# Performance work log

Measured on AMD Instinct MI355X. Metric: run time of the kernel, lower is better.

The kernel has to match this reference:

```python
import jax, jax.numpy as jnp
import numpy as np

INPUT, HIDDEN, OUTPUT = 128, 256, 128
BATCH, SEQ = 128, 2048


def setup_inputs() -> dict:
    key = jax.random.key(0)
    ks = jax.random.split(key, 6)
    s_in = 1.0 / np.sqrt(INPUT)
    s_h = 1.0 / np.sqrt(HIDDEN)
    return {
        "x": jax.random.normal(ks[0], (BATCH, SEQ, INPUT), dtype=jnp.float32),
        "W_in": jax.random.uniform(ks[1], (HIDDEN, INPUT), jnp.float32, -s_in, s_in),
        "b_in": jax.random.uniform(ks[2], (HIDDEN,), jnp.float32, -s_in, s_in),
        "W_rec": jax.random.uniform(ks[3], (HIDDEN, HIDDEN), jnp.float32, -s_h, s_h),
        "W_out": jax.random.uniform(ks[4], (OUTPUT, HIDDEN), jnp.float32, -s_h, s_h),
        "b_out": jax.random.uniform(ks[5], (OUTPUT,), jnp.float32, -s_h, s_h),
    }


def reference(x, W_in, b_in, W_rec, W_out, b_out):
    # Precompute input projection for all timesteps in one big GEMM: [B,S,H]
    xin = jnp.einsum("bsi,hi->bsh", x, W_in) + b_in

    def step(h, xin_t):
        # h: [B,H]; xin_t: [B,H]
        h_new = jax.nn.sigmoid(xin_t + h @ W_rec.T)
        return h_new, None

    h0 = jnp.zeros((x.shape[0], W_rec.shape[0]), dtype=x.dtype)
    h_final, _ = jax.lax.scan(step, h0, jnp.swapaxes(xin, 0, 1))  # scan over seq
    return h_final @ W_out.T + b_out  # [B, OUTPUT]
```

## Files before the change

kernel.cpp:

```cpp
#include <hip/hip_runtime.h>
#include <hip/hip_bf16.h>


#define BATCH 128
#define SEQ   2048
#define NIN   128
#define NH    256
#define NOUT  128

#define BTILE 16
#define NBLK  (BATCH / BTILE)
#define HPITCH 264
#define XPITCH 136
#define TCHUNK 16
#define LOG2E 1.4426950408889634f

typedef __attribute__((ext_vector_type(8))) short short8;
typedef __attribute__((ext_vector_type(4))) float f32x4;

__device__ __forceinline__ ushort f2bf(float f) {
    union { float f; uint u; } v; v.f = f;
    uint r = v.u + 0x7fffu + ((v.u >> 16) & 1u);
    return (ushort)(r >> 16);
}

__device__ __forceinline__ uint pk_bf16(float a, float b) {
    float2 p; p.x = a; p.y = b;
    __hip_bfloat162 h = __float22bfloat162_rn(p);
    union { __hip_bfloat162 h; uint u; } v; v.h = h; return v.u;
}

__device__ __forceinline__ short8 load_wfrag_s(const float* __restrict__ W, int ld,
                                               int row, int col, float scale) {
    const float4* p = (const float4*)(W + (size_t)row * ld + col);
    float4 a = p[0], b = p[1];
    union { short8 v; ushort u[8]; } r;
    r.u[0] = f2bf(a.x * scale); r.u[1] = f2bf(a.y * scale);
    r.u[2] = f2bf(a.z * scale); r.u[3] = f2bf(a.w * scale);
    r.u[4] = f2bf(b.x * scale); r.u[5] = f2bf(b.y * scale);
    r.u[6] = f2bf(b.z * scale); r.u[7] = f2bf(b.w * scale);
    return r.v;
}

__device__ __forceinline__ float bfhi2f(uint u) {
    union { uint u; float f; } v; v.u = u & 0xffff0000u; return v.f;
}
__device__ __forceinline__ float bflo2f(uint u) {
    union { uint u; float f; } v; v.u = u << 16; return v.f;
}

__global__ __launch_bounds__(256, 1)
void xin_gemm(const float* __restrict__ x,
              const float* __restrict__ W_in,
              const float* __restrict__ b_in,
              ushort* __restrict__ xin) {
    const int tid  = threadIdx.x;
    const int lane = tid & 63;
    const int wid  = tid >> 6;
    const int n15  = lane & 15;
    const int q    = lane >> 4;
    const int bblk = blockIdx.x * BTILE;
    const int t0   = blockIdx.y * TCHUNK;

    short8 win[4][4];
    float  bias[4][4];
    #pragma unroll
    for (int mt = 0; mt < 4; ++mt) {
        const int row = (wid * 4 + mt) * 16 + n15;
        #pragma unroll
        for (int kt = 0; kt < 4; ++kt)
            win[mt][kt] = load_wfrag_s(W_in, NIN, row, kt * 32 + q * 8, LOG2E);
        #pragma unroll
        for (int r = 0; r < 4; ++r)
            bias[mt][r] = LOG2E * b_in[(wid * 4 + mt) * 16 + q * 4 + r];
    }

    const size_t xrow = (size_t)(bblk + n15) * SEQ * NIN;

    #pragma unroll 1
    for (int tt = 0; tt < TCHUNK; ++tt) {
        const int t = t0 + tt;
        short8 bx[4];
        #pragma unroll
        for (int kt = 0; kt < 4; ++kt) {
            const float4* p = (const float4*)(x + xrow + (size_t)t * NIN + kt * 32 + q * 8);
            float4 a = p[0], b = p[1];
            union { short8 v; ushort u[8]; } r;
            r.u[0] = f2bf(a.x); r.u[1] = f2bf(a.y); r.u[2] = f2bf(a.z); r.u[3] = f2bf(a.w);
            r.u[4] = f2bf(b.x); r.u[5] = f2bf(b.y); r.u[6] = f2bf(b.z); r.u[7] = f2bf(b.w);
            bx[kt] = r.v;
        }
        f32x4 acc[4];
        #pragma unroll
        for (int mt = 0; mt < 4; ++mt) {
            acc[mt][0] = bias[mt][0]; acc[mt][1] = bias[mt][1];
            acc[mt][2] = bias[mt][2]; acc[mt][3] = bias[mt][3];
        }
        #pragma unroll
        for (int kt = 0; kt < 4; ++kt)
            #pragma unroll
            for (int mt = 0; mt < 4; ++mt)
                acc[mt] = __builtin_amdgcn_mfma_f32_16x16x32_bf16(
                    win[mt][kt], bx[kt], acc[mt], 0, 0, 0);
        #pragma unroll
        for (int mt = 0; mt < 4; ++mt) {
            uint2 w;
            w.x = pk_bf16(acc[mt][0], acc[mt][1]);
            w.y = pk_bf16(acc[mt][2], acc[mt][3]);
            *(uint2*)&xin[(size_t)t * BATCH * NH + (size_t)(bblk + n15) * NH
                          + (wid * 4 + mt) * 16 + q * 4] = w;
        }
    }
}

__global__ __launch_bounds__(512, 2)
void elman_scan(const ushort* __restrict__ xin,
                const float* __restrict__ W_rec,
                const float* __restrict__ W_out,
                const float* __restrict__ b_out,
                float* __restrict__ out) {
    const int tid  = threadIdx.x;
    const int lane = tid & 63;
    const int wid  = tid >> 6;
    const int n15  = lane & 15;
    const int q    = lane >> 4;
    const int bblk = blockIdx.x * BTILE;

    __shared__ __align__(16) ushort hlds[2][BTILE * HPITCH];

    short8 wrec[2][8];
    #pragma unroll
    for (int mt = 0; mt < 2; ++mt) {
        const int row = (wid * 2 + mt) * 16 + n15;
        #pragma unroll
        for (int kt = 0; kt < 8; ++kt)
            wrec[mt][kt] = load_wfrag_s(W_rec, NH, row, kt * 32 + q * 8, LOG2E);
    }

    for (int i = tid; i < BTILE * HPITCH / 2; i += 512)
        ((uint*)hlds[0])[i] = 0u;

    const size_t xoff = (size_t)(bblk + n15) * NH + q * 4;
    uint2 xin_cur[2], xin_nxt[2];
    #pragma unroll
    for (int mt = 0; mt < 2; ++mt)
        xin_cur[mt] = *(const uint2*)&xin[xoff + (wid * 2 + mt) * 16];

    __syncthreads();

    #pragma unroll 1
    for (int t = 0; t < SEQ; ++t) {
        const int cur = t & 1, nxt = cur ^ 1;

        const int tp = (t + 1 < SEQ) ? (t + 1) : (SEQ - 1);
        const size_t pb = (size_t)tp * BATCH * NH + xoff;
        #pragma unroll
        for (int mt = 0; mt < 2; ++mt)
            xin_nxt[mt] = *(const uint2*)&xin[pb + (wid * 2 + mt) * 16];

        short8 bh[8];
        #pragma unroll
        for (int kt = 0; kt < 8; ++kt)
            bh[kt] = *(const short8*)&hlds[cur][n15 * HPITCH + kt * 32 + q * 8];

        f32x4 acc[2];
        #pragma unroll
        for (int mt = 0; mt < 2; ++mt) {
            acc[mt][0] = bflo2f(xin_cur[mt].x);
            acc[mt][1] = bfhi2f(xin_cur[mt].x);
            acc[mt][2] = bflo2f(xin_cur[mt].y);
            acc[mt][3] = bfhi2f(xin_cur[mt].y);
        }
        #pragma unroll
        for (int kt = 0; kt < 8; ++kt)
            #pragma unroll
            for (int mt = 0; mt < 2; ++mt)
                acc[mt] = __builtin_amdgcn_mfma_f32_16x16x32_bf16(
                    wrec[mt][kt], bh[kt], acc[mt], 0, 0, 0);

        #pragma unroll
        for (int mt = 0; mt < 2; ++mt) {
            float h0 = __builtin_amdgcn_rcpf(1.0f + __builtin_amdgcn_exp2f(-acc[mt][0]));
            float h1 = __builtin_amdgcn_rcpf(1.0f + __builtin_amdgcn_exp2f(-acc[mt][1]));
            float h2 = __builtin_amdgcn_rcpf(1.0f + __builtin_amdgcn_exp2f(-acc[mt][2]));
            float h3 = __builtin_amdgcn_rcpf(1.0f + __builtin_amdgcn_exp2f(-acc[mt][3]));
            uint2 w;
            w.x = pk_bf16(h0, h1);
            w.y = pk_bf16(h2, h3);
            *(uint2*)&hlds[nxt][n15 * HPITCH + (wid * 2 + mt) * 16 + q * 4] = w;
        }

        #pragma unroll
        for (int mt = 0; mt < 2; ++mt) xin_cur[mt] = xin_nxt[mt];

        __syncthreads();
    }

    short8 wout[8];
    float  bo[4];
    {
        const int row = wid * 16 + n15;
        #pragma unroll
        for (int kt = 0; kt < 8; ++kt)
            wout[kt] = load_wfrag_s(W_out, NH, row, kt * 32 + q * 8, 1.0f);
        #pragma unroll
        for (int r = 0; r < 4; ++r)
            bo[r] = b_out[wid * 16 + q * 4 + r];
    }
    f32x4 oacc;
    oacc[0] = bo[0]; oacc[1] = bo[1]; oacc[2] = bo[2]; oacc[3] = bo[3];
    #pragma unroll
    for (int kt = 0; kt < 8; ++kt) {
        short8 bh = *(const short8*)&hlds[0][n15 * HPITCH + kt * 32 + q * 8];
        oacc = __builtin_amdgcn_mfma_f32_16x16x32_bf16(wout[kt], bh, oacc, 0, 0, 0);
    }
    #pragma unroll
    for (int r = 0; r < 4; ++r) {
        const int o = wid * 16 + q * 4 + r;
        out[(size_t)(bblk + n15) * NOUT + o] = oacc[r];
    }
}

__global__ __launch_bounds__(256, 1)
void elman_mfma(const float* __restrict__ x,
                const float* __restrict__ W_in,
                const float* __restrict__ b_in,
                const float* __restrict__ W_rec,
                const float* __restrict__ W_out,
                const float* __restrict__ b_out,
                float* __restrict__ out) {
    const int tid  = threadIdx.x;
    const int lane = tid & 63;
    const int wid  = tid >> 6;
    const int n15  = lane & 15;
    const int q    = lane >> 4;
    const int bblk = blockIdx.x * BTILE;

    __shared__ __align__(16) ushort hlds[2][BTILE * HPITCH];
    __shared__ __align__(16) ushort xlds[2][BTILE * XPITCH];

    short8 wrec[4][8];
    short8 win[4][4];
    float  bias[4][4];
    #pragma unroll
    for (int mt = 0; mt < 4; ++mt) {
        const int row = (wid * 4 + mt) * 16 + n15;
        #pragma unroll
        for (int kt = 0; kt < 8; ++kt)
            wrec[mt][kt] = load_wfrag_s(W_rec, NH, row, kt * 32 + q * 8, 1.0f);
        #pragma unroll
        for (int kt = 0; kt < 4; ++kt)
            win[mt][kt] = load_wfrag_s(W_in, NIN, row, kt * 32 + q * 8, 1.0f);
        #pragma unroll
        for (int r = 0; r < 4; ++r)
            bias[mt][r] = b_in[(wid * 4 + mt) * 16 + q * 4 + r];
    }

    for (int i = tid; i < BTILE * HPITCH / 2; i += 256)
        ((uint*)hlds[0])[i] = 0u;

    const int xr = tid >> 4;
    const int xc = (tid & 15) * 8;
    const size_t xbase = ((size_t)(bblk + xr)) * SEQ * NIN + xc;
    {
        const float4* p = (const float4*)(x + xbase);
        float4 a = p[0], b = p[1];
        union { uint4 u4; ushort s[8]; } px;
        px.s[0] = f2bf(a.x); px.s[1] = f2bf(a.y); px.s[2] = f2bf(a.z); px.s[3] = f2bf(a.w);
        px.s[4] = f2bf(b.x); px.s[5] = f2bf(b.y); px.s[6] = f2bf(b.z); px.s[7] = f2bf(b.w);
        *(uint4*)&xlds[0][xr * XPITCH + xc] = px.u4;
    }
    __syncthreads();

    #pragma unroll 1
    for (int t = 0; t < SEQ; ++t) {
        const int cur = t & 1, nxt = cur ^ 1;
        float4 xp0{}, xp1{};
        if (t + 1 < SEQ) {
            const float4* p = (const float4*)(x + xbase + (size_t)(t + 1) * NIN);
            xp0 = p[0]; xp1 = p[1];
        }
        short8 bx[4], bh[8];
        #pragma unroll
        for (int kt = 0; kt < 4; ++kt)
            bx[kt] = *(const short8*)&xlds[cur][n15 * XPITCH + kt * 32 + q * 8];
        #pragma unroll
        for (int kt = 0; kt < 8; ++kt)
            bh[kt] = *(const short8*)&hlds[cur][n15 * HPITCH + kt * 32 + q * 8];
        f32x4 acc[4];
        #pragma unroll
        for (int mt = 0; mt < 4; ++mt) {
            acc[mt][0] = bias[mt][0]; acc[mt][1] = bias[mt][1];
            acc[mt][2] = bias[mt][2]; acc[mt][3] = bias[mt][3];
        }
        #pragma unroll
        for (int kt = 0; kt < 4; ++kt)
            #pragma unroll
            for (int mt = 0; mt < 4; ++mt)
                acc[mt] = __builtin_amdgcn_mfma_f32_16x16x32_bf16(
                    win[mt][kt], bx[kt], acc[mt], 0, 0, 0);
        #pragma unroll
        for (int kt = 0; kt < 8; ++kt)
            #pragma unroll
            for (int mt = 0; mt < 4; ++mt)
                acc[mt] = __builtin_amdgcn_mfma_f32_16x16x32_bf16(
                    wrec[mt][kt], bh[kt], acc[mt], 0, 0, 0);
        #pragma unroll
        for (int mt = 0; mt < 4; ++mt) {
            float h0 = 1.0f / (1.0f + __expf(-acc[mt][0]));
            float h1 = 1.0f / (1.0f + __expf(-acc[mt][1]));
            float h2 = 1.0f / (1.0f + __expf(-acc[mt][2]));
            float h3 = 1.0f / (1.0f + __expf(-acc[mt][3]));
            uint2 w;
            w.x = pk_bf16(h0, h1);
            w.y = pk_bf16(h2, h3);
            *(uint2*)&hlds[nxt][n15 * HPITCH + (wid * 4 + mt) * 16 + q * 4] = w;
        }
        if (t + 1 < SEQ) {
            union { uint4 u4; ushort s[8]; } px;
            px.s[0] = f2bf(xp0.x); px.s[1] = f2bf(xp0.y);
            px.s[2] = f2bf(xp0.z); px.s[3] = f2bf(xp0.w);
            px.s[4] = f2bf(xp1.x); px.s[5] = f2bf(xp1.y);
            px.s[6] = f2bf(xp1.z); px.s[7] = f2bf(xp1.w);
            *(uint4*)&xlds[nxt][xr * XPITCH + xc] = px.u4;
        }
        __syncthreads();
    }

    short8 wout[2][8];
    float  bo[2][4];
    #pragma unroll
    for (int mo = 0; mo < 2; ++mo) {
        const int row = (wid * 2 + mo) * 16 + n15;
        #pragma unroll
        for (int kt = 0; kt < 8; ++kt)
            wout[mo][kt] = load_wfrag_s(W_out, NH, row, kt * 32 + q * 8, 1.0f);
        #pragma unroll
        for (int r = 0; r < 4; ++r)
            bo[mo][r] = b_out[(wid * 2 + mo) * 16 + q * 4 + r];
    }
    f32x4 oacc[2];
    #pragma unroll
    for (int mo = 0; mo < 2; ++mo) {
        oacc[mo][0] = bo[mo][0]; oacc[mo][1] = bo[mo][1];
        oacc[mo][2] = bo[mo][2]; oacc[mo][3] = bo[mo][3];
    }
    #pragma unroll
    for (int kt = 0; kt < 8; ++kt) {
        short8 bh = *(const short8*)&hlds[0][n15 * HPITCH + kt * 32 + q * 8];
        #pragma unroll
        for (int mo = 0; mo < 2; ++mo)
            oacc[mo] = __builtin_amdgcn_mfma_f32_16x16x32_bf16(
                wout[mo][kt], bh, oacc[mo], 0, 0, 0);
    }
    #pragma unroll
    for (int mo = 0; mo < 2; ++mo)
        #pragma unroll
        for (int r = 0; r < 4; ++r) {
            const int o = (wid * 2 + mo) * 16 + q * 4 + r;
            out[(size_t)(bblk + n15) * NOUT + o] = oacc[mo][r];
        }
}

extern "C" void kernel_launch(void* const* d_in, const int* in_sizes, int n_in,
                              void* d_out, int out_size, void* d_ws, size_t ws_size,
                              hipStream_t stream) {
    const float* x     = (const float*)d_in[0];
    const float* W_in  = (const float*)d_in[1];
    const float* b_in  = (const float*)d_in[2];
    const float* W_rec = (const float*)d_in[3];
    const float* W_out = (const float*)d_in[4];
    const float* b_out = (const float*)d_in[5];
    float* out = (float*)d_out;

    const size_t need = (size_t)SEQ * BATCH * NH * sizeof(ushort);
    if (ws_size >= need) {
        ushort* xin = (ushort*)d_ws;
        dim3 g1(NBLK, SEQ / TCHUNK);
        xin_gemm<<<g1, 256, 0, stream>>>(x, W_in, b_in, xin);
        elman_scan<<<NBLK, 512, 0, stream>>>(xin, W_rec, W_out, b_out, out);
    } else {
        elman_mfma<<<NBLK, 256, 0, stream>>>(x, W_in, b_in, W_rec, W_out, b_out, out);
    }
}
```

Baseline: 1.463 ms.

## Store xin in fragment-native layout and shrink scan block to four waves

The input-projection kernel now stages x through LDS with coalesced row loads and a double buffer. It writes xin in an MFMA-fragment-ordered layout so each lane of the scan kernel reads one contiguous uint2 per tile. The scan kernel drops from 8 to 4 waves per block, each owning 4 output tiles, which makes the per-step barrier cheaper. It also prefetches xin two steps ahead and replaces __syncthreads with a raw lgkmcnt wait plus s_barrier. In exchange, each wave does more serial MFMA work per step and holds more registers for W_rec fragments.

```diff
diff --git a/kernel.cpp b/kernel.cpp
--- a/kernel.cpp
+++ b/kernel.cpp
@@ -53,7 +53,7 @@
 void xin_gemm(const float* __restrict__ x,
               const float* __restrict__ W_in,
               const float* __restrict__ b_in,
-              ushort* __restrict__ xin) {
+              uint2* __restrict__ xin) {
     const int tid  = threadIdx.x;
     const int lane = tid & 63;
     const int wid  = tid >> 6;
@@ -62,6 +62,8 @@
     const int bblk = blockIdx.x * BTILE;
     const int t0   = blockIdx.y * TCHUNK;
 
+    __shared__ __align__(16) ushort xlds[2][BTILE * XPITCH];
+
     short8 win[4][4];
     float  bias[4][4];
     #pragma unroll
@@ -75,21 +77,35 @@
             bias[mt][r] = LOG2E * b_in[(wid * 4 + mt) * 16 + q * 4 + r];
     }
 
-    const size_t xrow = (size_t)(bblk + n15) * SEQ * NIN;
+    const int xr = tid >> 4;
+    const int xc = (tid & 15) * 8;
+    const size_t xbase = ((size_t)(bblk + xr)) * SEQ * NIN + xc;
+    {
+        const float4* p = (const float4*)(x + xbase + (size_t)t0 * NIN);
+        float4 a = p[0], b = p[1];
+        union { uint4 u4; ushort s[8]; } px;
+        px.s[0] = f2bf(a.x); px.s[1] = f2bf(a.y); px.s[2] = f2bf(a.z); px.s[3] = f2bf(a.w);
+        px.s[4] = f2bf(b.x); px.s[5] = f2bf(b.y); px.s[6] = f2bf(b.z); px.s[7] = f2bf(b.w);
+        *(uint4*)&xlds[0][xr * XPITCH + xc] = px.u4;
+    }
+    __syncthreads();
 
     #pragma unroll 1
     for (int tt = 0; tt < TCHUNK; ++tt) {
         const int t = t0 + tt;
+        const int cur = tt & 1, nxt = cur ^ 1;
+
+        float4 xp0{}, xp1{};
+        if (tt + 1 < TCHUNK) {
+            const float4* p = (const float4*)(x + xbase + (size_t)(t + 1) * NIN);
+            xp0 = p[0]; xp1 = p[1];
+        }
+
         short8 bx[4];
         #pragma unroll
-        for (int kt = 0; kt < 4; ++kt) {
-            const float4* p = (const float4*)(x + xrow + (size_t)t * NIN + kt * 32 + q * 8);
-            float4 a = p[0], b = p[1];
-            union { short8 v; ushort u[8]; } r;
-            r.u[0] = f2bf(a.x); r.u[1] = f2bf(a.y); r.u[2] = f2bf(a.z); r.u[3] = f2bf(a.w);
-            r.u[4] = f2bf(b.x); r.u[5] = f2bf(b.y); r.u[6] = f2bf(b.z); r.u[7] = f2bf(b.w);
-            bx[kt] = r.v;
-        }
+        for (int kt = 0; kt < 4; ++kt)
+            bx[kt] = *(const short8*)&xlds[cur][n15 * XPITCH + kt * 32 + q * 8];
+
         f32x4 acc[4];
         #pragma unroll
         for (int mt = 0; mt < 4; ++mt) {
@@ -102,19 +118,30 @@
             for (int mt = 0; mt < 4; ++mt)
                 acc[mt] = __builtin_amdgcn_mfma_f32_16x16x32_bf16(
                     win[mt][kt], bx[kt], acc[mt], 0, 0, 0);
+
+        const size_t tb = ((size_t)t * NBLK + blockIdx.x) * 16;
         #pragma unroll
         for (int mt = 0; mt < 4; ++mt) {
             uint2 w;
             w.x = pk_bf16(acc[mt][0], acc[mt][1]);
             w.y = pk_bf16(acc[mt][2], acc[mt][3]);
-            *(uint2*)&xin[(size_t)t * BATCH * NH + (size_t)(bblk + n15) * NH
-                          + (wid * 4 + mt) * 16 + q * 4] = w;
-        }
-    }
-}
-
-__global__ __launch_bounds__(512, 2)
-void elman_scan(const ushort* __restrict__ xin,
+            xin[(tb + wid * 4 + mt) * 64 + lane] = w;
+        }
+
+        if (tt + 1 < TCHUNK) {
+            union { uint4 u4; ushort s[8]; } px;
+            px.s[0] = f2bf(xp0.x); px.s[1] = f2bf(xp0.y);
+            px.s[2] = f2bf(xp0.z); px.s[3] = f2bf(xp0.w);
+            px.s[4] = f2bf(xp1.x); px.s[5] = f2bf(xp1.y);
+            px.s[6] = f2bf(xp1.z); px.s[7] = f2bf(xp1.w);
+            *(uint4*)&xlds[nxt][xr * XPITCH + xc] = px.u4;
+        }
+        __syncthreads();
+    }
+}
+
+__global__ __launch_bounds__(256, 1)
+void elman_scan(const uint2* __restrict__ xin,
                 const float* __restrict__ W_rec,
                 const float* __restrict__ W_out,
                 const float* __restrict__ b_out,
@@ -128,58 +155,64 @@
 
     __shared__ __align__(16) ushort hlds[2][BTILE * HPITCH];
 
-    short8 wrec[2][8];
-    #pragma unroll
-    for (int mt = 0; mt < 2; ++mt) {
-        const int row = (wid * 2 + mt) * 16 + n15;
+    short8 wrec[4][8];
+    #pragma unroll
+    for (int mt = 0; mt < 4; ++mt) {
+        const int row = (wid * 4 + mt) * 16 + n15;
         #pragma unroll
         for (int kt = 0; kt < 8; ++kt)
             wrec[mt][kt] = load_wfrag_s(W_rec, NH, row, kt * 32 + q * 8, LOG2E);
     }
 
-    for (int i = tid; i < BTILE * HPITCH / 2; i += 512)
+    for (int i = tid; i < BTILE * HPITCH / 2; i += 256)
         ((uint*)hlds[0])[i] = 0u;
 
-    const size_t xoff = (size_t)(bblk + n15) * NH + q * 4;
-    uint2 xin_cur[2], xin_nxt[2];
-    #pragma unroll
-    for (int mt = 0; mt < 2; ++mt)
-        xin_cur[mt] = *(const uint2*)&xin[xoff + (wid * 2 + mt) * 16];
+    const size_t TSTRIDE = (size_t)NBLK * 16 * 64;
+    const uint2* xb0 = xin + (size_t)blockIdx.x * 16 * 64 + (size_t)(wid * 4) * 64 + lane;
+
+    uint2 xa[4], xb[4];
+    #pragma unroll
+    for (int mt = 0; mt < 4; ++mt) xa[mt] = xb0[mt * 64];
+    #pragma unroll
+    for (int mt = 0; mt < 4; ++mt) xb[mt] = xb0[TSTRIDE + mt * 64];
 
     __syncthreads();
 
-    #pragma unroll 1
-    for (int t = 0; t < SEQ; ++t) {
+    const int hbase = n15 * HPITCH;
+
+    auto step = [&](int t, uint2 (&X)[4]) {
         const int cur = t & 1, nxt = cur ^ 1;
 
-        const int tp = (t + 1 < SEQ) ? (t + 1) : (SEQ - 1);
-        const size_t pb = (size_t)tp * BATCH * NH + xoff;
-        #pragma unroll
-        for (int mt = 0; mt < 2; ++mt)
-            xin_nxt[mt] = *(const uint2*)&xin[pb + (wid * 2 + mt) * 16];
-
         short8 bh[8];
         #pragma unroll
         for (int kt = 0; kt < 8; ++kt)
-            bh[kt] = *(const short8*)&hlds[cur][n15 * HPITCH + kt * 32 + q * 8];
-
-        f32x4 acc[2];
-        #pragma unroll
-        for (int mt = 0; mt < 2; ++mt) {
-            acc[mt][0] = bflo2f(xin_cur[mt].x);
-            acc[mt][1] = bfhi2f(xin_cur[mt].x);
-            acc[mt][2] = bflo2f(xin_cur[mt].y);
-            acc[mt][3] = bfhi2f(xin_cur[mt].y);
-        }
-        #pragma unroll
-        for (int kt = 0; kt < 8; ++kt)
+            bh[kt] = *(const short8*)&hlds[cur][hbase + kt * 32 + q * 8];
+
+        f32x4 acc[4];
+        #pragma unroll
+        for (int mt = 0; mt < 4; ++mt) {
+            acc[mt][0] = bflo2f(X[mt].x);
+            acc[mt][1] = bfhi2f(X[mt].x);
+            acc[mt][2] = bflo2f(X[mt].y);
+            acc[mt][3] = bfhi2f(X[mt].y);
+        }
+
+        {
+            const int tp = (t + 2 < SEQ) ? (t + 2) : (SEQ - 1);
+            const uint2* p = xb0 + (size_t)tp * TSTRIDE;
             #pragma unroll
-            for (int mt = 0; mt < 2; ++mt)
+            for (int mt = 0; mt < 4; ++mt) X[mt] = p[mt * 64];
+        }
+
+        #pragma unroll
+        for (int kt = 0; kt < 8; ++kt)
+            #pragma unroll
+            for (int mt = 0; mt < 4; ++mt)
                 acc[mt] = __builtin_amdgcn_mfma_f32_16x16x32_bf16(
                     wrec[mt][kt], bh[kt], acc[mt], 0, 0, 0);
 
         #pragma unroll
-        for (int mt = 0; mt < 2; ++mt) {
+        for (int mt = 0; mt < 4; ++mt) {
             float h0 = __builtin_amdgcn_rcpf(1.0f + __builtin_amdgcn_exp2f(-acc[mt][0]));
             float h1 = __builtin_amdgcn_rcpf(1.0f + __builtin_amdgcn_exp2f(-acc[mt][1]));
             float h2 = __builtin_amdgcn_rcpf(1.0f + __builtin_amdgcn_exp2f(-acc[mt][2]));
@@ -187,38 +220,51 @@
             uint2 w;
             w.x = pk_bf16(h0, h1);
             w.y = pk_bf16(h2, h3);
-            *(uint2*)&hlds[nxt][n15 * HPITCH + (wid * 2 + mt) * 16 + q * 4] = w;
-        }
-
-        #pragma unroll
-        for (int mt = 0; mt < 2; ++mt) xin_cur[mt] = xin_nxt[mt];
-
-        __syncthreads();
-    }
-
-    short8 wout[8];
-    float  bo[4];
-    {
-        const int row = wid * 16 + n15;
-        #pragma unroll
-        for (int kt = 0; kt < 8; ++kt)
-            wout[kt] = load_wfrag_s(W_out, NH, row, kt * 32 + q * 8, 1.0f);
+            *(uint2*)&hlds[nxt][hbase + (wid * 4 + mt) * 16 + q * 4] = w;
+        }
+
+        asm volatile("s_waitcnt lgkmcnt(0)" ::: "memory");
+        __builtin_amdgcn_s_barrier();
+    };
+
+    #pragma unroll 1
+    for (int t = 0; t < SEQ; t += 2) {
+        step(t, xa);
+        step(t + 1, xb);
+    }
+
+    short8 wout[2][8];
+    float  bo[2][4];
+    #pragma unroll
+    for (int mo = 0; mo < 2; ++mo) {
+        const int row = (wid * 2 + mo) * 16 + n15;
+        #pragma unroll
+        for (int kt = 0; kt < 8; ++kt)
+            wout[mo][kt] = load_wfrag_s(W_out, NH, row, kt * 32 + q * 8, 1.0f);
         #pragma unroll
         for (int r = 0; r < 4; ++r)
-            bo[r] = b_out[wid * 16 + q * 4 + r];
-    }
-    f32x4 oacc;
-    oacc[0] = bo[0]; oacc[1] = bo[1]; oacc[2] = bo[2]; oacc[3] = bo[3];
+            bo[mo][r] = b_out[(wid * 2 + mo) * 16 + q * 4 + r];
+    }
+    f32x4 oacc[2];
+    #pragma unroll
+    for (int mo = 0; mo < 2; ++mo) {
+        oacc[mo][0] = bo[mo][0]; oacc[mo][1] = bo[mo][1];
+        oacc[mo][2] = bo[mo][2]; oacc[mo][3] = bo[mo][3];
+    }
     #pragma unroll
     for (int kt = 0; kt < 8; ++kt) {
-        short8 bh = *(const short8*)&hlds[0][n15 * HPITCH + kt * 32 + q * 8];
-        oacc = __builtin_amdgcn_mfma_f32_16x16x32_bf16(wout[kt], bh, oacc, 0, 0, 0);
-    }
-    #pragma unroll
-    for (int r = 0; r < 4; ++r) {
-        const int o = wid * 16 + q * 4 + r;
-        out[(size_t)(bblk + n15) * NOUT + o] = oacc[r];
-    }
+        short8 bh = *(const short8*)&hlds[0][hbase + kt * 32 + q * 8];
+        #pragma unroll
+        for (int mo = 0; mo < 2; ++mo)
+            oacc[mo] = __builtin_amdgcn_mfma_f32_16x16x32_bf16(wout[mo][kt], bh, oacc[mo], 0, 0, 0);
+    }
+    #pragma unroll
+    for (int mo = 0; mo < 2; ++mo)
+        #pragma unroll
+        for (int r = 0; r < 4; ++r) {
+            const int o = (wid * 2 + mo) * 16 + q * 4 + r;
+            out[(size_t)(bblk + n15) * NOUT + o] = oacc[mo][r];
+        }
 }
 
 __global__ __launch_bounds__(256, 1)
@@ -375,10 +421,10 @@
 
     const size_t need = (size_t)SEQ * BATCH * NH * sizeof(ushort);
     if (ws_size >= need) {
-        ushort* xin = (ushort*)d_ws;
+        uint2* xin = (uint2*)d_ws;
         dim3 g1(NBLK, SEQ / TCHUNK);
         xin_gemm<<<g1, 256, 0, stream>>>(x, W_in, b_in, xin);
-        elman_scan<<<NBLK, 512, 0, stream>>>(xin, W_rec, W_out, b_out, out);
+        elman_scan<<<NBLK, 256, 0, stream>>>(xin, W_rec, W_out, b_out, out);
     } else {
         elman_mfma<<<NBLK, 256, 0, stream>>>(x, W_in, b_in, W_rec, W_out, b_out, out);
     }
```

New measurement: 1.579 ms. +8.0%, slower.

## Store xin and hidden state in MFMA fragment-native layout, deepen prefetch

Applied to the files above, without the earlier changes.

The precomputed input projection is now written in a fragment-ordered layout, so each lane of the scan kernel reads one contiguous uint2 per tile, and consecutive lanes hit consecutive addresses. The hidden-state shared buffer is also reorganised into fragment-native uint2 slots. This changes the bank-conflict pattern and the index math on the serial critical path. The scan loop is unrolled by two with a two-step-ahead global prefetch, and __syncthreads is replaced by an explicit lgkmcnt wait plus s_barrier. The GEMM kernel also halves its time chunk and raises its occupancy hint.

```diff
diff --git a/kernel.cpp b/kernel.cpp
--- a/kernel.cpp
+++ b/kernel.cpp
@@ -12,7 +12,7 @@
 #define NBLK  (BATCH / BTILE)
 #define HPITCH 264
 #define XPITCH 136
-#define TCHUNK 16
+#define TCHUNK 8
 #define LOG2E 1.4426950408889634f
 
 typedef __attribute__((ext_vector_type(8))) short short8;
@@ -49,11 +49,11 @@
     union { uint u; float f; } v; v.u = u << 16; return v.f;
 }
 
-__global__ __launch_bounds__(256, 1)
+__global__ __launch_bounds__(256, 2)
 void xin_gemm(const float* __restrict__ x,
               const float* __restrict__ W_in,
               const float* __restrict__ b_in,
-              ushort* __restrict__ xin) {
+              uint2* __restrict__ xin) {
     const int tid  = threadIdx.x;
     const int lane = tid & 63;
     const int wid  = tid >> 6;
@@ -75,15 +75,15 @@
             bias[mt][r] = LOG2E * b_in[(wid * 4 + mt) * 16 + q * 4 + r];
     }
 
-    const size_t xrow = (size_t)(bblk + n15) * SEQ * NIN;
+    const float* xrow = x + ((size_t)(bblk + n15) * SEQ + t0) * NIN + q * 8;
 
     #pragma unroll 1
     for (int tt = 0; tt < TCHUNK; ++tt) {
-        const int t = t0 + tt;
+        const float* xp = xrow + (size_t)tt * NIN;
         short8 bx[4];
         #pragma unroll
         for (int kt = 0; kt < 4; ++kt) {
-            const float4* p = (const float4*)(x + xrow + (size_t)t * NIN + kt * 32 + q * 8);
+            const float4* p = (const float4*)(xp + kt * 32);
             float4 a = p[0], b = p[1];
             union { short8 v; ushort u[8]; } r;
             r.u[0] = f2bf(a.x); r.u[1] = f2bf(a.y); r.u[2] = f2bf(a.z); r.u[3] = f2bf(a.w);
@@ -102,19 +102,20 @@
             for (int mt = 0; mt < 4; ++mt)
                 acc[mt] = __builtin_amdgcn_mfma_f32_16x16x32_bf16(
                     win[mt][kt], bx[kt], acc[mt], 0, 0, 0);
+
+        const size_t tb = ((size_t)(t0 + tt) * NBLK + blockIdx.x) * 16;
         #pragma unroll
         for (int mt = 0; mt < 4; ++mt) {
             uint2 w;
             w.x = pk_bf16(acc[mt][0], acc[mt][1]);
             w.y = pk_bf16(acc[mt][2], acc[mt][3]);
-            *(uint2*)&xin[(size_t)t * BATCH * NH + (size_t)(bblk + n15) * NH
-                          + (wid * 4 + mt) * 16 + q * 4] = w;
+            xin[(tb + wid * 4 + mt) * 64 + lane] = w;
         }
     }
 }
 
 __global__ __launch_bounds__(512, 2)
-void elman_scan(const ushort* __restrict__ xin,
+void elman_scan(const uint2* __restrict__ xin,
                 const float* __restrict__ W_rec,
                 const float* __restrict__ W_out,
                 const float* __restrict__ b_out,
@@ -126,7 +127,7 @@
     const int q    = lane >> 4;
     const int bblk = blockIdx.x * BTILE;
 
-    __shared__ __align__(16) ushort hlds[2][BTILE * HPITCH];
+    __shared__ __align__(16) uint2 hlds[2][16 * 64];
 
     short8 wrec[2][8];
     #pragma unroll
@@ -137,40 +138,50 @@
             wrec[mt][kt] = load_wfrag_s(W_rec, NH, row, kt * 32 + q * 8, LOG2E);
     }
 
-    for (int i = tid; i < BTILE * HPITCH / 2; i += 512)
-        ((uint*)hlds[0])[i] = 0u;
-
-    const size_t xoff = (size_t)(bblk + n15) * NH + q * 4;
-    uint2 xin_cur[2], xin_nxt[2];
-    #pragma unroll
-    for (int mt = 0; mt < 2; ++mt)
-        xin_cur[mt] = *(const uint2*)&xin[xoff + (wid * 2 + mt) * 16];
+    for (int i = tid; i < 16 * 64; i += 512) {
+        uint2 z; z.x = 0u; z.y = 0u;
+        hlds[0][i] = z;
+    }
+
+    const size_t TSTRIDE = (size_t)NBLK * 16 * 64;
+    const uint2* xb0 = xin + (size_t)blockIdx.x * 16 * 64 + (size_t)(wid * 2) * 64 + lane;
+
+    uint2 xa[2], xb[2];
+    #pragma unroll
+    for (int mt = 0; mt < 2; ++mt) xa[mt] = xb0[mt * 64];
+    #pragma unroll
+    for (int mt = 0; mt < 2; ++mt) xb[mt] = xb0[TSTRIDE + mt * 64];
 
     __syncthreads();
 
-    #pragma unroll 1
-    for (int t = 0; t < SEQ; ++t) {
+    const int rbase = n15 * 4 + 2 * (q & 1);
+    const int shalf = q >> 1;
+    const int woff  = n15 * 4 + q;
+
+    auto step = [&](int t, uint2 (&X)[2]) {
         const int cur = t & 1, nxt = cur ^ 1;
 
-        const int tp = (t + 1 < SEQ) ? (t + 1) : (SEQ - 1);
-        const size_t pb = (size_t)tp * BATCH * NH + xoff;
-        #pragma unroll
-        for (int mt = 0; mt < 2; ++mt)
-            xin_nxt[mt] = *(const uint2*)&xin[pb + (wid * 2 + mt) * 16];
-
         short8 bh[8];
         #pragma unroll
         for (int kt = 0; kt < 8; ++kt)
-            bh[kt] = *(const short8*)&hlds[cur][n15 * HPITCH + kt * 32 + q * 8];
+            bh[kt] = *(const short8*)&hlds[cur][(2 * kt + shalf) * 64 + rbase];
 
         f32x4 acc[2];
         #pragma unroll
         for (int mt = 0; mt < 2; ++mt) {
-            acc[mt][0] = bflo2f(xin_cur[mt].x);
-            acc[mt][1] = bfhi2f(xin_cur[mt].x);
-            acc[mt][2] = bflo2f(xin_cur[mt].y);
-            acc[mt][3] = bfhi2f(xin_cur[mt].y);
-        }
+            acc[mt][0] = bflo2f(X[mt].x);
+            acc[mt][1] = bfhi2f(X[mt].x);
+            acc[mt][2] = bflo2f(X[mt].y);
+            acc[mt][3] = bfhi2f(X[mt].y);
+        }
+
+        {
+            const int tp = (t + 2 < SEQ) ? (t + 2) : (SEQ - 1);
+            const uint2* p = xb0 + (size_t)tp * TSTRIDE;
+            #pragma unroll
+            for (int mt = 0; mt < 2; ++mt) X[mt] = p[mt * 64];
+        }
+
         #pragma unroll
         for (int kt = 0; kt < 8; ++kt)
             #pragma unroll
@@ -187,13 +198,17 @@
             uint2 w;
             w.x = pk_bf16(h0, h1);
             w.y = pk_bf16(h2, h3);
-            *(uint2*)&hlds[nxt][n15 * HPITCH + (wid * 2 + mt) * 16 + q * 4] = w;
-        }
-
-        #pragma unroll
-        for (int mt = 0; mt < 2; ++mt) xin_cur[mt] = xin_nxt[mt];
-
-        __syncthreads();
+            hlds[nxt][(wid * 2 + mt) * 64 + woff] = w;
+        }
+
+        asm volatile("s_waitcnt lgkmcnt(0)" ::: "memory");
+        __builtin_amdgcn_s_barrier();
+    };
+
+    #pragma unroll 1
+    for (int t = 0; t < SEQ; t += 2) {
+        step(t, xa);
+        step(t + 1, xb);
     }
 
     short8 wout[8];
@@ -211,7 +226,7 @@
     oacc[0] = bo[0]; oacc[1] = bo[1]; oacc[2] = bo[2]; oacc[3] = bo[3];
     #pragma unroll
     for (int kt = 0; kt < 8; ++kt) {
-        short8 bh = *(const short8*)&hlds[0][n15 * HPITCH + kt * 32 + q * 8];
+        short8 bh = *(const short8*)&hlds[0][(2 * kt + shalf) * 64 + rbase];
         oacc = __builtin_amdgcn_mfma_f32_16x16x32_bf16(wout[kt], bh, oacc, 0, 0, 0);
     }
     #pragma unroll
@@ -375,7 +390,7 @@
 
     const size_t need = (size_t)SEQ * BATCH * NH * sizeof(ushort);
     if (ws_size >= need) {
-        ushort* xin = (ushort*)d_ws;
+        uint2* xin = (uint2*)d_ws;
         dim3 g1(NBLK, SEQ / TCHUNK);
         xin_gemm<<<g1, 256, 0, stream>>>(x, W_in, b_in, xin);
         elman_scan<<<NBLK, 512, 0, stream>>>(xin, W_rec, W_out, b_out, out);
```

Measured after the change: 1.365 ms. 6.7% less time.
